# Kernel tuning notes

Measured on AMD Instinct MI355X. Metric: run time of the kernel, lower is better.

The kernel has to match this reference:

```python
import jax, jax.numpy as jnp
import numpy as np

B, T, D = 4, 2048, 1024
H = 16
DH = D // H
BASE = 10000.0


def _rope_tables(seq_len, dim):
    inv_freq = 1.0 / (BASE ** (np.arange(0, dim, 2, dtype=np.float32) / dim))
    pos = np.arange(seq_len, dtype=np.float32)
    freqs = np.outer(pos, inv_freq)            # (T, dim/2)
    emb = np.concatenate([freqs, freqs], -1)   # (T, dim)
    return jnp.asarray(np.cos(emb)), jnp.asarray(np.sin(emb))


def setup_inputs() -> dict:
    key = jax.random.key(0)
    ks = jax.random.split(key, 5)
    s = 1.0 / np.sqrt(D)
    x = jax.random.normal(ks[0], (B, T, D), jnp.float32)
    Wqkv = jax.random.normal(ks[1], (D, 3 * D), jnp.float32) * s
    bqkv = jnp.zeros((3 * D,), jnp.float32)
    Wproj = jax.random.normal(ks[2], (D, D), jnp.float32) * s
    bproj = jnp.zeros((D,), jnp.float32)
    cos, sin = _rope_tables(T, DH)
    return {"x": x, "Wqkv": Wqkv, "bqkv": bqkv, "Wproj": Wproj,
            "bproj": bproj, "cos": cos, "sin": sin}


def _rotate_half(u):
    u1, u2 = jnp.split(u, 2, axis=-1)
    return jnp.concatenate([-u2, u1], axis=-1)


def reference(x, Wqkv, bqkv, Wproj, bproj, cos, sin):
    b, t, d = x.shape
    qkv = x @ Wqkv + bqkv                       # (B, T, 3D)
    qkv = qkv.reshape(b, t, 3, H, DH)           # matches '(three h d)' order
    q, k, v = qkv[:, :, 0], qkv[:, :, 1], qkv[:, :, 2]  # (B, T, H, DH)
    c = cos[None, :, None, :]                   # (1, T, 1, DH)
    s = sin[None, :, None, :]
    q = q * c + _rotate_half(q) * s
    k = k * c + _rotate_half(k) * s
    scale = DH ** -0.5
    attn = jnp.einsum('bthd,bshd->bhts', q, k) * scale   # (B, H, T, T)
    attn = jax.nn.softmax(attn, axis=-1)
    out = jnp.einsum('bhts,bshd->bthd', attn, v)          # (B, T, H, DH)
    out = out.reshape(b, t, d)
    return out @ Wproj + bproj
```

## Files before the change

kernel.cpp:

```cpp
#include <hip/hip_runtime.h>


typedef _Float16 half_t;
typedef _Float16 half8 __attribute__((ext_vector_type(8)));
typedef _Float16 half4v __attribute__((ext_vector_type(4)));
typedef float floatx4 __attribute__((ext_vector_type(4)));

#define MFMA_F16 __builtin_amdgcn_mfma_f32_16x16x32_f16

constexpr int Bdim = 4, T = 2048, D = 1024, H = 16, DH = 64;
constexpr int Mrows = Bdim * T;
constexpr int N1 = 3 * D;
constexpr int KD = D;

constexpr float QSCALE = 0.125f * 1.4426950408889634f;
constexpr float CSHIFT = 4.0f * 1.4426950408889634f;

__device__ __forceinline__ void gl_lds16(const half_t* g, half_t* l) {
  __builtin_amdgcn_global_load_lds(
      (const __attribute__((address_space(1))) void*)g,
      (__attribute__((address_space(3))) void*)l, 16, 0, 0);
}

__global__ __launch_bounds__(256) void cvt_kernel(const float* __restrict__ s,
                                                  half_t* __restrict__ d, int n4) {
  int i = blockIdx.x * 256 + threadIdx.x;
  if (i < n4) {
    float4 v = ((const float4*)s)[i];
    half4v h;
    h[0] = (half_t)v.x; h[1] = (half_t)v.y; h[2] = (half_t)v.z; h[3] = (half_t)v.w;
    ((half4v*)d)[i] = h;
  }
}

__global__ __launch_bounds__(64) void cvt_transpose(const float* __restrict__ W,
                                                    half_t* __restrict__ Wt,
                                                    int Kr, int Nc) {
  __shared__ half_t Th[32][36];
  const int l = threadIdx.x;
  const int n0 = blockIdx.x * 32, k0 = blockIdx.y * 32;
#pragma unroll
  for (int i = 0; i < 4; ++i) {
    int kk = (l >> 3) + i * 8;
    int nn4 = (l & 7) * 4;
    float4 v = *(const float4*)(W + (size_t)(k0 + kk) * Nc + n0 + nn4);
    half4v h;
    h[0] = (half_t)v.x; h[1] = (half_t)v.y; h[2] = (half_t)v.z; h[3] = (half_t)v.w;
    *(half4v*)&Th[kk][nn4] = h;
  }
  __syncthreads();
#pragma unroll
  for (int i = 0; i < 4; ++i) {
    int nn = (l >> 3) + i * 8;
    int kk4 = (l & 7) * 4;
    half4v h;
#pragma unroll
    for (int j = 0; j < 4; ++j) h[j] = Th[kk4 + j][nn];
    *(half4v*)(Wt + (size_t)(n0 + nn) * Kr + k0 + kk4) = h;
  }
}

__global__ __launch_bounds__(256) void gemm_qkv_rope(
    const half_t* __restrict__ X, const half_t* __restrict__ Wt,
    const float* __restrict__ bias, const float* __restrict__ cosT,
    const float* __restrict__ sinT,
    half_t* __restrict__ Q, half_t* __restrict__ K, half_t* __restrict__ V) {
  __shared__ half_t As[128 * 32];
  __shared__ half_t Bs[128 * 32];
  const int tid = threadIdx.x;
  const int lane = tid & 63, wv = tid >> 6;
  const int wm = wv >> 1, wn = wv & 1;
  const int qd = lane >> 4, ln = lane & 15;
  const int bn = blockIdx.x, bm = blockIdx.y;

  floatx4 acc[4][4] = {};

  for (int k0 = 0; k0 < KD; k0 += 32) {
#pragma unroll
    for (int p = 0; p < 2; ++p) {
      int c = tid + p * 256;
      int row = c >> 2, col = (c & 3) << 3;
      gl_lds16(X + (size_t)(bm * 128 + row) * KD + k0 + col, As + c * 8);
      gl_lds16(Wt + (size_t)(bn * 128 + row) * KD + k0 + col, Bs + c * 8);
    }
    __syncthreads();

    half8 af[4], bf[4];
#pragma unroll
    for (int mi = 0; mi < 4; ++mi)
      af[mi] = *(const half8*)&As[(wm * 64 + mi * 16 + ln) * 32 + qd * 8];
#pragma unroll
    for (int ni = 0; ni < 4; ++ni)
      bf[ni] = *(const half8*)&Bs[(wn * 64 + ni * 16 + ln) * 32 + qd * 8];
#pragma unroll
    for (int mi = 0; mi < 4; ++mi)
#pragma unroll
      for (int ni = 0; ni < 4; ++ni)
        acc[mi][ni] = MFMA_F16(af[mi], bf[ni], acc[mi][ni], 0, 0, 0);
    __syncthreads();
  }

  const int n0 = bn * 128 + wn * 64;
  const int sreg = n0 >> 10;
  const int h = (n0 & 1023) >> 6;
  float bv[4];
#pragma unroll
  for (int ni = 0; ni < 4; ++ni) bv[ni] = bias[n0 + ni * 16 + ln];

  if (sreg == 2) {
#pragma unroll
    for (int mi = 0; mi < 4; ++mi) {
      int m0 = bm * 128 + wm * 64 + mi * 16 + qd * 4;
      int b = m0 >> 11, t0 = m0 & (T - 1);
#pragma unroll
      for (int ni = 0; ni < 4; ++ni) {
        int dh = ni * 16 + ln;
        half4v hv;
#pragma unroll
        for (int r = 0; r < 4; ++r) hv[r] = (half_t)(acc[mi][ni][r] + bv[ni]);
        *(half4v*)(V + ((size_t)(b * H + h) * DH + dh) * T + t0) = hv;
      }
    }
  } else {
    const float qscale = (sreg == 0) ? QSCALE : 1.0f;
    half_t* OUT = (sreg == 0) ? Q : K;
#pragma unroll
    for (int mi = 0; mi < 4; ++mi) {
#pragma unroll
      for (int r = 0; r < 4; ++r) {
        int m = bm * 128 + wm * 64 + mi * 16 + qd * 4 + r;
        int b = m >> 11, t = m & (T - 1);
        float v0 = acc[mi][0][r] + bv[0];
        float v1 = acc[mi][1][r] + bv[1];
        float v2 = acc[mi][2][r] + bv[2];
        float v3 = acc[mi][3][r] + bv[3];
        float c0 = cosT[t * 64 + ln],      s0 = sinT[t * 64 + ln];
        float c1 = cosT[t * 64 + 16 + ln], s1 = sinT[t * 64 + 16 + ln];
        float c2 = cosT[t * 64 + 32 + ln], s2 = sinT[t * 64 + 32 + ln];
        float c3 = cosT[t * 64 + 48 + ln], s3 = sinT[t * 64 + 48 + ln];
        float o0 = v0 * c0 - v2 * s0;
        float o1 = v1 * c1 - v3 * s1;
        float o2 = v2 * c2 + v0 * s2;
        float o3 = v3 * c3 + v1 * s3;
        size_t base = ((size_t)(b * H + h) * T + t) * DH;
        OUT[base + 0 * 16 + ln] = (half_t)(o0 * qscale);
        OUT[base + 1 * 16 + ln] = (half_t)(o1 * qscale);
        OUT[base + 2 * 16 + ln] = (half_t)(o2 * qscale);
        OUT[base + 3 * 16 + ln] = (half_t)(o3 * qscale);
      }
    }
  }
}

__global__ __launch_bounds__(256) void flash_attn(
    const half_t* __restrict__ Q, const half_t* __restrict__ K,
    const half_t* __restrict__ Vt, half_t* __restrict__ AO) {
  __shared__ __align__(16) half_t Klds[64 * 64];
  __shared__ __align__(16) half_t Vlds[64 * 64];
  const int tid = threadIdx.x;
  const int lane = tid & 63, wv = tid >> 6;
  const int qd = lane >> 4, ln = lane & 15;
  const int bh = blockIdx.y;
  const int q0 = blockIdx.x * 256 + wv * 64;
  const half_t* Qb = Q + (size_t)bh * T * DH;
  const half_t* Kb = K + (size_t)bh * T * DH;
  const half_t* Vb = Vt + (size_t)bh * DH * T;

  const int sr0 = tid >> 3, sc0 = (tid & 7) << 3;
  const int sr1 = sr0 + 32;
  const int so0 = sr0 * 64 + (sc0 ^ ((sr0 & 7) << 3));
  const int so1 = sr1 * 64 + (sc0 ^ ((sr1 & 7) << 3));

  half8 qf[4][2];
#pragma unroll
  for (int mi = 0; mi < 4; ++mi)
#pragma unroll
    for (int ks = 0; ks < 2; ++ks)
      qf[mi][ks] = *(const half8*)(Qb + (size_t)(q0 + mi * 16 + ln) * DH + ks * 32 + qd * 8);

  floatx4 Oacc[4][4] = {};
  float Ls[4] = {0.f, 0.f, 0.f, 0.f};

  for (int s0 = 0; s0 < T; s0 += 64) {
    *(half8*)&Klds[so0] = *(const half8*)(Kb + (size_t)(s0 + sr0) * DH + sc0);
    *(half8*)&Klds[so1] = *(const half8*)(Kb + (size_t)(s0 + sr1) * DH + sc0);
    *(half8*)&Vlds[so0] = *(const half8*)(Vb + (size_t)sr0 * T + s0 + sc0);
    *(half8*)&Vlds[so1] = *(const half8*)(Vb + (size_t)sr1 * T + s0 + sc0);
    __syncthreads();

#pragma unroll
    for (int ko = 0; ko < 2; ++ko) {
      half8 kf[2][2];
#pragma unroll
      for (int ks = 0; ks < 2; ++ks)
#pragma unroll
        for (int par = 0; par < 2; ++par) {
          int krow = ko * 32 + 2 * ln + par;
          kf[ks][par] = *(const half8*)&Klds[krow * 64 + (((ks * 32) | (qd * 8)) ^ ((krow & 7) << 3))];
        }

      half8 pf[4];
#pragma unroll
      for (int mi = 0; mi < 4; ++mi) {
        floatx4 s4[2];
#pragma unroll
        for (int par = 0; par < 2; ++par)
          s4[par] = (floatx4){-CSHIFT, -CSHIFT, -CSHIFT, -CSHIFT};
#pragma unroll
        for (int ks = 0; ks < 2; ++ks)
#pragma unroll
          for (int par = 0; par < 2; ++par)
            s4[par] = MFMA_F16(kf[ks][par], qf[mi][ks], s4[par], 0, 0, 0);
#pragma unroll
        for (int r = 0; r < 4; ++r) {
          float pe = __builtin_amdgcn_exp2f(s4[0][r]);
          float po = __builtin_amdgcn_exp2f(s4[1][r]);
          Ls[mi] += pe + po;
          pf[mi][2 * r]     = (half_t)pe;
          pf[mi][2 * r + 1] = (half_t)po;
        }
      }

#pragma unroll
      for (int di = 0; di < 4; ++di) {
        int vrow = di * 16 + ln;
        half8 vf = *(const half8*)&Vlds[vrow * 64 + (((ko * 32) | (qd * 8)) ^ ((vrow & 7) << 3))];
#pragma unroll
        for (int mi = 0; mi < 4; ++mi)
          Oacc[mi][di] = MFMA_F16(pf[mi], vf, Oacc[mi][di], 0, 0, 0);
      }
    }
    __syncthreads();
  }

#pragma unroll
  for (int mi = 0; mi < 4; ++mi) {
    Ls[mi] += __shfl_xor(Ls[mi], 16);
    Ls[mi] += __shfl_xor(Ls[mi], 32);
  }

  const int b = bh >> 4, h = bh & 15;
#pragma unroll
  for (int mi = 0; mi < 4; ++mi) {
#pragma unroll
    for (int r = 0; r < 4; ++r) {
      float invL = 1.f / __shfl(Ls[mi], qd * 4 + r);
      int t = q0 + mi * 16 + qd * 4 + r;
      size_t base = ((size_t)b * T + t) * D + h * DH;
#pragma unroll
      for (int di = 0; di < 4; ++di)
        AO[base + di * 16 + ln] = (half_t)(Oacc[mi][di][r] * invL);
    }
  }
}

__global__ __launch_bounds__(256) void gemm_proj(
    const half_t* __restrict__ X, const half_t* __restrict__ Wt,
    const float* __restrict__ bias, float* __restrict__ OUTF) {
  __shared__ half_t As[128 * 32];
  __shared__ half_t Bs[128 * 32];
  const int tid = threadIdx.x;
  const int lane = tid & 63, wv = tid >> 6;
  const int wm = wv >> 1, wn = wv & 1;
  const int qd = lane >> 4, ln = lane & 15;
  const int bn = blockIdx.x, bm = blockIdx.y;

  floatx4 acc[4][4] = {};

  for (int k0 = 0; k0 < KD; k0 += 32) {
#pragma unroll
    for (int p = 0; p < 2; ++p) {
      int c = tid + p * 256;
      int row = c >> 2, col = (c & 3) << 3;
      gl_lds16(X + (size_t)(bm * 128 + row) * KD + k0 + col, As + c * 8);
      gl_lds16(Wt + (size_t)(bn * 128 + row) * KD + k0 + col, Bs + c * 8);
    }
    __syncthreads();

    half8 af[4], bf[4];
#pragma unroll
    for (int mi = 0; mi < 4; ++mi)
      af[mi] = *(const half8*)&As[(wm * 64 + mi * 16 + ln) * 32 + qd * 8];
#pragma unroll
    for (int ni = 0; ni < 4; ++ni)
      bf[ni] = *(const half8*)&Bs[(wn * 64 + ni * 16 + ln) * 32 + qd * 8];
#pragma unroll
    for (int mi = 0; mi < 4; ++mi)
#pragma unroll
      for (int ni = 0; ni < 4; ++ni)
        acc[mi][ni] = MFMA_F16(af[mi], bf[ni], acc[mi][ni], 0, 0, 0);
    __syncthreads();
  }

  const int n0 = bn * 128 + wn * 64;
  float bv[4];
#pragma unroll
  for (int ni = 0; ni < 4; ++ni) bv[ni] = bias[n0 + ni * 16 + ln];
#pragma unroll
  for (int mi = 0; mi < 4; ++mi) {
#pragma unroll
    for (int r = 0; r < 4; ++r) {
      int m = bm * 128 + wm * 64 + mi * 16 + qd * 4 + r;
#pragma unroll
      for (int ni = 0; ni < 4; ++ni)
        OUTF[(size_t)m * D + n0 + ni * 16 + ln] = acc[mi][ni][r] + bv[ni];
    }
  }
}

extern "C" void kernel_launch(void* const* d_in, const int* in_sizes, int n_in,
                              void* d_out, int out_size, void* d_ws, size_t ws_size,
                              hipStream_t stream) {
  const float* x     = (const float*)d_in[0];
  const float* Wqkv  = (const float*)d_in[1];
  const float* bqkv  = (const float*)d_in[2];
  const float* Wproj = (const float*)d_in[3];
  const float* bproj = (const float*)d_in[4];
  const float* cosT  = (const float*)d_in[5];
  const float* sinT  = (const float*)d_in[6];
  float* out = (float*)d_out;

  half_t* xh      = (half_t*)d_ws;
  half_t* Wqkvt   = xh + (size_t)Mrows * KD;
  half_t* Wprojt  = Wqkvt + (size_t)KD * N1;
  half_t* Qb      = Wprojt + (size_t)D * D;
  half_t* Kb      = Qb + (size_t)Bdim * H * T * DH;
  half_t* Vb      = Kb + (size_t)Bdim * H * T * DH;
  half_t* AO      = xh;

  cvt_kernel<<<(Mrows * KD / 4 + 255) / 256, 256, 0, stream>>>(x, xh, Mrows * KD / 4);
  cvt_transpose<<<dim3(N1 / 32, KD / 32), 64, 0, stream>>>(Wqkv, Wqkvt, KD, N1);
  cvt_transpose<<<dim3(D / 32, KD / 32), 64, 0, stream>>>(Wproj, Wprojt, KD, D);

  gemm_qkv_rope<<<dim3(N1 / 128, Mrows / 128), 256, 0, stream>>>(
      xh, Wqkvt, bqkv, cosT, sinT, Qb, Kb, Vb);
  flash_attn<<<dim3(T / 256, Bdim * H), 256, 0, stream>>>(Qb, Kb, Vb, AO);
  gemm_proj<<<dim3(D / 128, Mrows / 128), 256, 0, stream>>>(AO, Wprojt, bproj, out);
}
```

Measured before the change: 320.7 us.

## Double-buffer flash attention tiles, MFMA row sums, transposed RoPE tables, swapped grid

Flash attention now prefetches the next K/V tile into registers while computing on the current LDS buffer, using two LDS buffers so only one barrier per tile is needed. Softmax row sums are computed with an MFMA against a ones vector instead of scalar adds and cross-lane shuffles. A new kernel transposes the cos/sin tables so the QKV epilogue can load them as float4 vectors. The attention grid is reordered so consecutive blocks cover different heads. This adds LDS usage and an extra small launch, and the extra MFMA per tile adds matrix work.

```diff
diff --git a/kernel.cpp b/kernel.cpp
--- a/kernel.cpp
+++ b/kernel.cpp
@@ -33,6 +33,16 @@
   }
 }
 
+__global__ __launch_bounds__(256) void cs_transpose(const float* __restrict__ c,
+                                                    const float* __restrict__ s,
+                                                    float* __restrict__ ct,
+                                                    float* __restrict__ st) {
+  int i = blockIdx.x * 256 + threadIdx.x;
+  int dh = i >> 11, t = i & (T - 1);
+  ct[i] = c[t * 64 + dh];
+  st[i] = s[t * 64 + dh];
+}
+
 __global__ __launch_bounds__(64) void cvt_transpose(const float* __restrict__ W,
                                                     half_t* __restrict__ Wt,
                                                     int Kr, int Nc) {
@@ -62,8 +72,8 @@
 
 __global__ __launch_bounds__(256) void gemm_qkv_rope(
     const half_t* __restrict__ X, const half_t* __restrict__ Wt,
-    const float* __restrict__ bias, const float* __restrict__ cosT,
-    const float* __restrict__ sinT,
+    const float* __restrict__ bias, const float* __restrict__ cosTt,
+    const float* __restrict__ sinTt,
     half_t* __restrict__ Q, half_t* __restrict__ K, half_t* __restrict__ V) {
   __shared__ half_t As[128 * 32];
   __shared__ half_t Bs[128 * 32];
@@ -126,22 +136,25 @@
     half_t* OUT = (sreg == 0) ? Q : K;
 #pragma unroll
     for (int mi = 0; mi < 4; ++mi) {
+      int m0 = bm * 128 + wm * 64 + mi * 16 + qd * 4;
+      int b = m0 >> 11, t0 = m0 & (T - 1);
+      float4 cc[4], ss[4];
+#pragma unroll
+      for (int k = 0; k < 4; ++k) {
+        cc[k] = *(const float4*)(cosTt + (size_t)(k * 16 + ln) * T + t0);
+        ss[k] = *(const float4*)(sinTt + (size_t)(k * 16 + ln) * T + t0);
+      }
 #pragma unroll
       for (int r = 0; r < 4; ++r) {
-        int m = bm * 128 + wm * 64 + mi * 16 + qd * 4 + r;
-        int b = m >> 11, t = m & (T - 1);
+        int t = t0 + r;
         float v0 = acc[mi][0][r] + bv[0];
         float v1 = acc[mi][1][r] + bv[1];
         float v2 = acc[mi][2][r] + bv[2];
         float v3 = acc[mi][3][r] + bv[3];
-        float c0 = cosT[t * 64 + ln],      s0 = sinT[t * 64 + ln];
-        float c1 = cosT[t * 64 + 16 + ln], s1 = sinT[t * 64 + 16 + ln];
-        float c2 = cosT[t * 64 + 32 + ln], s2 = sinT[t * 64 + 32 + ln];
-        float c3 = cosT[t * 64 + 48 + ln], s3 = sinT[t * 64 + 48 + ln];
-        float o0 = v0 * c0 - v2 * s0;
-        float o1 = v1 * c1 - v3 * s1;
-        float o2 = v2 * c2 + v0 * s2;
-        float o3 = v3 * c3 + v1 * s3;
+        float o0 = v0 * ((const float*)&cc[0])[r] - v2 * ((const float*)&ss[0])[r];
+        float o1 = v1 * ((const float*)&cc[1])[r] - v3 * ((const float*)&ss[1])[r];
+        float o2 = v2 * ((const float*)&cc[2])[r] + v0 * ((const float*)&ss[2])[r];
+        float o3 = v3 * ((const float*)&cc[3])[r] + v1 * ((const float*)&ss[3])[r];
         size_t base = ((size_t)(b * H + h) * T + t) * DH;
         OUT[base + 0 * 16 + ln] = (half_t)(o0 * qscale);
         OUT[base + 1 * 16 + ln] = (half_t)(o1 * qscale);
@@ -155,13 +168,13 @@
 __global__ __launch_bounds__(256) void flash_attn(
     const half_t* __restrict__ Q, const half_t* __restrict__ K,
     const half_t* __restrict__ Vt, half_t* __restrict__ AO) {
-  __shared__ __align__(16) half_t Klds[64 * 64];
-  __shared__ __align__(16) half_t Vlds[64 * 64];
+  __shared__ __align__(16) half_t Klds[2][64 * 64];
+  __shared__ __align__(16) half_t Vlds[2][64 * 64];
   const int tid = threadIdx.x;
   const int lane = tid & 63, wv = tid >> 6;
   const int qd = lane >> 4, ln = lane & 15;
-  const int bh = blockIdx.y;
-  const int q0 = blockIdx.x * 256 + wv * 64;
+  const int bh = blockIdx.x;
+  const int q0 = blockIdx.y * 256 + wv * 64;
   const half_t* Qb = Q + (size_t)bh * T * DH;
   const half_t* Kb = K + (size_t)bh * T * DH;
   const half_t* Vb = Vt + (size_t)bh * DH * T;
@@ -179,14 +192,31 @@
       qf[mi][ks] = *(const half8*)(Qb + (size_t)(q0 + mi * 16 + ln) * DH + ks * 32 + qd * 8);
 
   floatx4 Oacc[4][4] = {};
-  float Ls[4] = {0.f, 0.f, 0.f, 0.f};
-
-  for (int s0 = 0; s0 < T; s0 += 64) {
-    *(half8*)&Klds[so0] = *(const half8*)(Kb + (size_t)(s0 + sr0) * DH + sc0);
-    *(half8*)&Klds[so1] = *(const half8*)(Kb + (size_t)(s0 + sr1) * DH + sc0);
-    *(half8*)&Vlds[so0] = *(const half8*)(Vb + (size_t)sr0 * T + s0 + sc0);
-    *(half8*)&Vlds[so1] = *(const half8*)(Vb + (size_t)sr1 * T + s0 + sc0);
-    __syncthreads();
+  floatx4 Lacc[4] = {};
+  half8 ones;
+#pragma unroll
+  for (int j = 0; j < 8; ++j) ones[j] = (half_t)1.0f;
+
+  half8 kp0 = *(const half8*)(Kb + (size_t)sr0 * DH + sc0);
+  half8 kp1 = *(const half8*)(Kb + (size_t)sr1 * DH + sc0);
+  half8 vp0 = *(const half8*)(Vb + (size_t)sr0 * T + sc0);
+  half8 vp1 = *(const half8*)(Vb + (size_t)sr1 * T + sc0);
+  *(half8*)&Klds[0][so0] = kp0; *(half8*)&Klds[0][so1] = kp1;
+  *(half8*)&Vlds[0][so0] = vp0; *(half8*)&Vlds[0][so1] = vp1;
+  __syncthreads();
+
+  int cur = 0;
+  for (int it = 0; it < T / 64; ++it) {
+    const bool more = (it + 1) < (T / 64);
+    if (more) {
+      int s1 = (it + 1) * 64;
+      kp0 = *(const half8*)(Kb + (size_t)(s1 + sr0) * DH + sc0);
+      kp1 = *(const half8*)(Kb + (size_t)(s1 + sr1) * DH + sc0);
+      vp0 = *(const half8*)(Vb + (size_t)sr0 * T + s1 + sc0);
+      vp1 = *(const half8*)(Vb + (size_t)sr1 * T + s1 + sc0);
+    }
+    const half_t* Kl = Klds[cur];
+    const half_t* Vl = Vlds[cur];
 
 #pragma unroll
     for (int ko = 0; ko < 2; ++ko) {
@@ -196,7 +226,7 @@
 #pragma unroll
         for (int par = 0; par < 2; ++par) {
           int krow = ko * 32 + 2 * ln + par;
-          kf[ks][par] = *(const half8*)&Klds[krow * 64 + (((ks * 32) | (qd * 8)) ^ ((krow & 7) << 3))];
+          kf[ks][par] = *(const half8*)&Kl[krow * 64 + (((ks * 32) | (qd * 8)) ^ ((krow & 7) << 3))];
         }
 
       half8 pf[4];
@@ -215,7 +245,6 @@
         for (int r = 0; r < 4; ++r) {
           float pe = __builtin_amdgcn_exp2f(s4[0][r]);
           float po = __builtin_amdgcn_exp2f(s4[1][r]);
-          Ls[mi] += pe + po;
           pf[mi][2 * r]     = (half_t)pe;
           pf[mi][2 * r + 1] = (half_t)po;
         }
@@ -224,27 +253,31 @@
 #pragma unroll
       for (int di = 0; di < 4; ++di) {
         int vrow = di * 16 + ln;
-        half8 vf = *(const half8*)&Vlds[vrow * 64 + (((ko * 32) | (qd * 8)) ^ ((vrow & 7) << 3))];
+        half8 vf = *(const half8*)&Vl[vrow * 64 + (((ko * 32) | (qd * 8)) ^ ((vrow & 7) << 3))];
 #pragma unroll
         for (int mi = 0; mi < 4; ++mi)
           Oacc[mi][di] = MFMA_F16(pf[mi], vf, Oacc[mi][di], 0, 0, 0);
       }
-    }
-    __syncthreads();
-  }
-
+#pragma unroll
+      for (int mi = 0; mi < 4; ++mi)
+        Lacc[mi] = MFMA_F16(pf[mi], ones, Lacc[mi], 0, 0, 0);
+    }
+
+    if (more) {
+      int nxt = cur ^ 1;
+      *(half8*)&Klds[nxt][so0] = kp0; *(half8*)&Klds[nxt][so1] = kp1;
+      *(half8*)&Vlds[nxt][so0] = vp0; *(half8*)&Vlds[nxt][so1] = vp1;
+      __syncthreads();
+      cur = nxt;
+    }
+  }
+
+  const int b = bh >> 4, h = bh & 15;
 #pragma unroll
   for (int mi = 0; mi < 4; ++mi) {
-    Ls[mi] += __shfl_xor(Ls[mi], 16);
-    Ls[mi] += __shfl_xor(Ls[mi], 32);
-  }
-
-  const int b = bh >> 4, h = bh & 15;
-#pragma unroll
-  for (int mi = 0; mi < 4; ++mi) {
 #pragma unroll
     for (int r = 0; r < 4; ++r) {
-      float invL = 1.f / __shfl(Ls[mi], qd * 4 + r);
+      float invL = 1.f / Lacc[mi][r];
       int t = q0 + mi * 16 + qd * 4 + r;
       size_t base = ((size_t)b * T + t) * D + h * DH;
 #pragma unroll
@@ -326,14 +359,17 @@
   half_t* Qb      = Wprojt + (size_t)D * D;
   half_t* Kb      = Qb + (size_t)Bdim * H * T * DH;
   half_t* Vb      = Kb + (size_t)Bdim * H * T * DH;
+  float*  cosTt   = (float*)(Vb + (size_t)Bdim * H * T * DH);
+  float*  sinTt   = cosTt + (size_t)DH * T;
   half_t* AO      = xh;
 
   cvt_kernel<<<(Mrows * KD / 4 + 255) / 256, 256, 0, stream>>>(x, xh, Mrows * KD / 4);
   cvt_transpose<<<dim3(N1 / 32, KD / 32), 64, 0, stream>>>(Wqkv, Wqkvt, KD, N1);
   cvt_transpose<<<dim3(D / 32, KD / 32), 64, 0, stream>>>(Wproj, Wprojt, KD, D);
+  cs_transpose<<<(DH * T + 255) / 256, 256, 0, stream>>>(cosT, sinT, cosTt, sinTt);
 
   gemm_qkv_rope<<<dim3(N1 / 128, Mrows / 128), 256, 0, stream>>>(
-      xh, Wqkvt, bqkv, cosT, sinT, Qb, Kb, Vb);
-  flash_attn<<<dim3(T / 256, Bdim * H), 256, 0, stream>>>(Qb, Kb, Vb, AO);
+      xh, Wqkvt, bqkv, cosTt, sinTt, Qb, Kb, Vb);
+  flash_attn<<<dim3(Bdim * H, T / 256), 256, 0, stream>>>(Qb, Kb, Vb, AO);
   gemm_proj<<<dim3(D / 128, Mrows / 128), 256, 0, stream>>>(AO, Wprojt, bproj, out);
 }
```

Result: no change. 323.8 us (+1.0%).
